# Optimization experiments

Measured on AMD Instinct MI355X. Metric: run time of the kernel, lower is better.

Reference implementation:

```python
import jax, jax.numpy as jnp
import numpy as np
from jax import lax

MAX_BOXES = 1000
IOU_THRESHOLD = 0.5
SCORE_THRESHOLD = 0.3
N_BOXES = 300000
N_FEAT = 85  # 4 box + 1 conf + 80 classes


def setup_inputs() -> dict:
    key = jax.random.key(0)
    inputs = jax.random.uniform(key, (N_BOXES, N_FEAT), dtype=jnp.float32)
    return {"inputs": inputs}


def _nms_indices(boxes, scores, max_boxes, iou_thr):
    """Fixed-size greedy NMS (tf.image.non_max_suppression semantics).
    Returns (idxs[max_boxes] int32, valid[max_boxes] bool). Padded slots invalid.
    Indices are non-differentiable, matching TF."""
    boxes = lax.stop_gradient(boxes)
    scores = lax.stop_gradient(scores)
    y1, x1, y2, x2 = boxes[:, 0], boxes[:, 1], boxes[:, 2], boxes[:, 3]
    areas = (y2 - y1) * (x2 - x1)

    def step(cur_scores, _):
        idx = jnp.argmax(cur_scores)
        valid = jnp.isfinite(cur_scores[idx])
        b = boxes[idx]
        iy1 = jnp.maximum(b[0], y1)
        ix1 = jnp.maximum(b[1], x1)
        iy2 = jnp.minimum(b[2], y2)
        ix2 = jnp.minimum(b[3], x2)
        inter = jnp.maximum(iy2 - iy1, 0.0) * jnp.maximum(ix2 - ix1, 0.0)
        union = areas[idx] + areas - inter
        iou = jnp.where(union > 0, inter / union, 0.0)
        suppress = (iou > iou_thr) & valid
        new_scores = jnp.where(suppress, -jnp.inf, cur_scores)
        new_scores = new_scores.at[idx].set(-jnp.inf)
        return new_scores, (idx.astype(jnp.int32), valid)

    _, (idxs, valids) = lax.scan(step, scores, None, length=max_boxes)
    return idxs, valids


def reference(inputs):
    boxes = inputs[..., 0:4]                      # [N,4]
    box_confidence = inputs[..., 4:5]             # [N,1]
    box_class_probs = inputs[..., 5:]             # [N,C]
    box_scores = box_confidence * box_class_probs # [N,C]
    box_classes = jnp.argmax(box_scores, axis=-1)        # [N]
    box_class_scores = jnp.max(box_scores, axis=-1)      # [N]
    # boolean_mask emulated by sending failing scores to -inf (fixed shape)
    keep = box_class_scores >= SCORE_THRESHOLD
    masked_scores = jnp.where(keep, box_class_scores, -jnp.inf)

    idxs, valids = _nms_indices(boxes, masked_scores, MAX_BOXES, IOU_THRESHOLD)

    out_boxes = boxes[idxs]                                  # [max_boxes,4]
    out_scores = box_class_scores[idxs][:, None]             # [max_boxes,1]
    out_classes = box_classes[idxs].astype(jnp.float32)[:, None]
    out = jnp.concatenate([out_boxes, out_classes, out_scores], axis=-1)  # [max_boxes,6]
    # zero padded (invalid) rows; original returned variable-length [k,6]
    return jnp.where(valids[:, None], out, 0.0)
```

## Files before the change

kernel.cpp:

```cpp
#include <hip/hip_runtime.h>

#define NBOX 300000
#define NFEAT 85
#define NCLS 80
#define NBUCK 4096
#define HSPLIT 16
#define CMAX 8192
#define W64 (CMAX / 64)
#define MAXKEEP 1000
#define SC_ROWS 64

typedef unsigned long long u64;
typedef float f4a __attribute__((ext_vector_type(4), aligned(16)));

__device__ __forceinline__ int bucket_of(float s) {
    int b = (int)((s - 0.3f) * (4096.0f / 0.7f));
    if (b < 0) b = 0;
    if (b > NBUCK - 1) b = NBUCK - 1;
    return b;
}

__device__ __forceinline__ bool sup_iou(float by1, float bx1, float by2, float bx2, float ba,
                                        float y1, float x1, float y2, float x2, float area) {
    float iy1 = fmaxf(by1, y1), ix1 = fmaxf(bx1, x1);
    float iy2 = fminf(by2, y2), ix2 = fminf(bx2, x2);
    float inter = fmaxf(iy2 - iy1, 0.0f) * fmaxf(ix2 - ix1, 0.0f);
    float uni = ba + area - inter;
    float iou = (uni > 0.0f) ? inter / uni : 0.0f;
    return iou > 0.5f;
}

__global__ void k_init(unsigned* __restrict__ hist16, unsigned* __restrict__ cnt,
                       int* __restrict__ meta) {
    int i = blockIdx.x * blockDim.x + threadIdx.x;
    if (i < HSPLIT * NBUCK) hist16[i] = 0u;
    if (i < NBUCK) cnt[i] = 0u;
    if (i < 16) meta[i] = 0;
}

__global__ void __launch_bounds__(256) k_scores(const float* __restrict__ in,
        float* __restrict__ scores, unsigned* __restrict__ hist16) {
    __shared__ float lds[SC_ROWS * NFEAT];
    int t = threadIdx.x;
    long long rbase = (long long)blockIdx.x * SC_ROWS;
    int rows = (NBOX - rbase < SC_ROWS) ? (int)(NBOX - rbase) : SC_ROWS;
    int nfl = rows * NFEAT;
    int nf4 = nfl >> 2;
    const f4a* src = (const f4a*)(in + rbase * NFEAT);
    f4a* dst = (f4a*)lds;
    for (int k = t; k < nf4; k += 256) dst[k] = src[k];
    for (int k = (nf4 << 2) + t; k < nfl; k += 256) lds[k] = in[rbase * NFEAT + k];
    __syncthreads();
    unsigned* myhist = hist16 + (size_t)(blockIdx.x & (HSPLIT - 1)) * NBUCK;
    int row = t >> 2, part = t & 3;
    if (row < rows) {
        const float* r = lds + row * NFEAT;
        const float* p = r + 5 + 20 * part;
        float mx = p[0];
        #pragma unroll
        for (int j = 1; j < 20; ++j) mx = fmaxf(mx, p[j]);
        mx = fmaxf(mx, __shfl_xor(mx, 1));
        mx = fmaxf(mx, __shfl_xor(mx, 2));
        if (part == 0) {
            float best = r[4] * mx;
            scores[rbase + row] = best;
            if (best >= 0.3f) atomicAdd(&myhist[bucket_of(best)], 1u);
        }
    }
}

__global__ void __launch_bounds__(1024) k_thresh(const unsigned* __restrict__ hist16,
        unsigned* __restrict__ histsum, unsigned* __restrict__ off, int* __restrict__ meta) {
    __shared__ unsigned chunk[1024];
    int t = threadIdx.x;
    unsigned h[4];
    unsigned s = 0;
    #pragma unroll
    for (int j = 0; j < 4; ++j) {
        unsigned v = 0;
        for (int g = 0; g < HSPLIT; ++g) v += hist16[g * NBUCK + t * 4 + j];
        h[j] = v; histsum[t * 4 + j] = v; s += v;
    }
    chunk[t] = s;
    __syncthreads();
    for (int o = 1; o < 1024; o <<= 1) {
        unsigned add = (t + o < 1024) ? chunk[t + o] : 0u;
        __syncthreads();
        chunk[t] += add;
        __syncthreads();
    }
    unsigned after = (t + 1 < 1024) ? chunk[t + 1] : 0u;
    unsigned suf[5];
    suf[4] = after;
    #pragma unroll
    for (int j = 3; j >= 0; --j) suf[j] = suf[j + 1] + h[j];
    #pragma unroll
    for (int j = 0; j < 4; ++j) {
        int b = t * 4 + j;
        off[b] = suf[j] - h[j];
        unsigned sufb = suf[j];
        unsigned sufprev;
        if (b == 0) sufprev = 0xFFFFFFFFu;
        else if (j > 0) sufprev = suf[j - 1];
        else {
            unsigned hprev = 0;
            for (int g = 0; g < HSPLIT; ++g) hprev += hist16[g * NBUCK + b - 1];
            sufprev = sufb + hprev;
        }
        if (sufb <= (unsigned)CMAX && sufprev > (unsigned)CMAX) {
            meta[1] = b;
            meta[0] = (int)sufb;
        }
    }
}

__global__ void k_scatter(const float* __restrict__ scores, const int* __restrict__ meta,
                          const unsigned* __restrict__ off, unsigned* __restrict__ cnt,
                          u64* __restrict__ unsorted) {
    int i = blockIdx.x * blockDim.x + threadIdx.x;
    if (i >= NBOX) return;
    float s = scores[i];
    if (s < 0.3f) return;
    int b = bucket_of(s);
    if (b < meta[1]) return;
    unsigned slot = off[b] + atomicAdd(&cnt[b], 1u);
    if (slot < CMAX)
        unsorted[slot] = ((u64)__float_as_uint(s) << 32) |
                         (u64)(0xFFFFFFFFu - (unsigned)i);
}

__global__ void k_rank(const float* __restrict__ in, const u64* __restrict__ unsorted,
                       const unsigned* __restrict__ off, const unsigned* __restrict__ histsum,
                       const int* __restrict__ meta, u64* __restrict__ sorted,
                       float4* __restrict__ boxes4, unsigned* __restrict__ vflag) {
    int i = blockIdx.x * blockDim.x + threadIdx.x;
    int total = meta[0];
    if (i >= total) return;
    u64 k = unsorted[i];
    float s = __uint_as_float((unsigned)(k >> 32));
    int b = bucket_of(s);
    unsigned base = off[b];
    unsigned n = histsum[b];
    unsigned r = 0;
    for (unsigned u = 0; u < n; ++u) r += (unsorted[base + u] > k) ? 1u : 0u;
    int bi = (int)(0xFFFFFFFFu - (unsigned)(k & 0xFFFFFFFFull));
    const float* p = in + (size_t)bi * NFEAT;
    float4 bx = make_float4(p[0], p[1], p[2], p[3]);
    sorted[base + r] = k;
    boxes4[base + r] = bx;
    vflag[base + r] = (bx.z > bx.x && bx.w > bx.y) ? 1u : 0u;
}

__global__ void __launch_bounds__(1024) k_vscan(const unsigned* __restrict__ vflag,
        const float4* __restrict__ boxes4, int* __restrict__ meta,
        unsigned* __restrict__ vincl, unsigned* __restrict__ cmap,
        float4* __restrict__ cboxes) {
    __shared__ unsigned ps[1024];
    int t = threadIdx.x;
    int total = meta[0];
    unsigned f[8];
    unsigned run = 0;
    #pragma unroll
    for (int e = 0; e < 8; ++e) {
        int s = t * 8 + e;
        unsigned v = (s < total) ? vflag[s] : 0u;
        run += v;
        f[e] = run;
    }
    ps[t] = run;
    __syncthreads();
    for (int o = 1; o < 1024; o <<= 1) {
        unsigned add = (t >= o) ? ps[t - o] : 0u;
        __syncthreads();
        ps[t] += add;
        __syncthreads();
    }
    unsigned excl = (t > 0) ? ps[t - 1] : 0u;
    #pragma unroll
    for (int e = 0; e < 8; ++e) {
        int s = t * 8 + e;
        unsigned incl = excl + f[e];
        vincl[s] = incl;
        if (s < total && vflag[s]) {
            cmap[incl - 1] = (unsigned)s;
            cboxes[incl - 1] = boxes4[s];
        }
    }
    if (t == 1023) meta[3] = (int)ps[1023];
}

__global__ void __launch_bounds__(256) k_masks(const float4* __restrict__ cboxes,
        const int* __restrict__ meta, u64* __restrict__ masks) {
    int ti = blockIdx.y, tj = blockIdx.x;
    if (tj < ti) return;
    int count = meta[3];
    if (ti * 64 >= count) return;
    __shared__ float4 rb[64];
    int t = threadIdx.x;
    if (t < 64) {
        int r = ti * 64 + t;
        rb[t] = (r < count) ? cboxes[r] : make_float4(0.f, 0.f, 0.f, 0.f);
    }
    int lane = t & 63, wid = t >> 6;
    int cj = tj * 64 + lane;
    bool cvalid = (cj < count);
    float4 cb = cvalid ? cboxes[cj] : make_float4(0.f, 0.f, 0.f, 0.f);
    float carea = (cb.z - cb.x) * (cb.w - cb.y);
    __syncthreads();
    #pragma unroll
    for (int r = 0; r < 16; ++r) {
        int i = ti * 64 + wid * 16 + r;
        float4 b = rb[wid * 16 + r];
        float ba = (b.z - b.x) * (b.w - b.y);
        bool s = cvalid && (cj > i) && (i < count) &&
                 sup_iou(b.x, b.y, b.z, b.w, ba, cb.x, cb.y, cb.z, cb.w, carea);
        u64 word = __ballot(s ? 1 : 0);
        if (lane == 0) masks[(size_t)i * W64 + tj] = word;
    }
}

__global__ void __launch_bounds__(1024) k_sweepfin(const u64* __restrict__ masks,
        const unsigned* __restrict__ cmap, const unsigned* __restrict__ vincl,
        const unsigned* __restrict__ vflag, int* __restrict__ meta,
        int* __restrict__ kfinal) {
    __shared__ __align__(16) u64 stage[2][64][130];
    __shared__ u64 vkeptw[W64];
    __shared__ unsigned ps[1024];
    __shared__ int sh_wlim;
    int t = threadIdx.x;
    if (t < W64) vkeptw[t] = 0ull;
    if (t == 0) sh_wlim = 0;
    __syncthreads();
    int total = meta[0];
    int nv = meta[3];

    if (t < 64) {
        int lane = t;
        int nblkv = (nv + 63) >> 6;
        u64 r0 = 0ull, r1 = 0ull;
        int nkv = 0, wl = 0;

        if (nblkv > 0) {
            #pragma unroll
            for (int k = 0; k < 64; ++k)
                __builtin_amdgcn_global_load_lds(
                    (const __attribute__((address_space(1))) void*)(masks + (size_t)k * W64 + 2 * lane),
                    (__attribute__((address_space(3))) void*)&stage[0][k][0], 16, 0, 0);
        }

        for (int w = 0; w < nblkv; ++w) {
            int buf = w & 1;
            int base = w << 6;
            int rc = nv - base;
            u64 vm = (rc >= 64) ? ~0ull : ((1ull << rc) - 1ull);
            u64 rw = __shfl((w & 1) ? r1 : r0, w >> 1);
            u64 surv = ~rw & vm;
            int cend = (base + 63 < nv - 1) ? (base + 63) : (nv - 1);
            unsigned cm = cmap[cend];
            bool more = (w + 1 < nblkv);
            int base2 = base + 64;

            if (more) {
                #pragma unroll
                for (int k = 0; k < 32; ++k)
                    __builtin_amdgcn_global_load_lds(
                        (const __attribute__((address_space(1))) void*)(masks + (size_t)(base2 + k) * W64 + 2 * lane),
                        (__attribute__((address_space(3))) void*)&stage[buf ^ 1][k][0], 16, 0, 0);
                asm volatile("s_waitcnt vmcnt(32)" ::: "memory");
            } else {
                asm volatile("s_waitcnt vmcnt(0)" ::: "memory");
            }
            __builtin_amdgcn_sched_barrier(0);

            u64 diag_cur = stage[buf][lane][w];
            u64 Z = __ballot(diag_cur == 0ull);
            u64 rem = 0ull;
            u64 mnz = surv & ~Z;
            while (mnz) {
                int b = __ffsll(mnz) - 1;
                mnz &= mnz - 1;
                if ((rem >> b) & 1ull) continue;
                u64 db = __shfl(diag_cur, b);
                rem |= db;
                mnz &= ~db;
            }
            u64 kept = surv & ~rem;
            int kp = __popcll(kept);

            if (more) {
                #pragma unroll
                for (int k = 32; k < 64; ++k)
                    __builtin_amdgcn_global_load_lds(
                        (const __attribute__((address_space(1))) void*)(masks + (size_t)(base2 + k) * W64 + 2 * lane),
                        (__attribute__((address_space(3))) void*)&stage[buf ^ 1][k][0], 16, 0, 0);
            }

            {
                u64 km = kept;
                u64 alo = 0ull, ahi = 0ull;
                while (km) {
                    int b = __ffsll(km) - 1;
                    km &= km - 1;
                    alo |= stage[buf][b][2 * lane];
                    ahi |= stage[buf][b][2 * lane + 1];
                }
                r0 |= alo; r1 |= ahi;
            }
            if (lane == 0) vkeptw[w] = kept;
            nkv += kp;
            wl = w + 1;
            if ((int)cm - cend + nkv >= MAXKEEP) break;
        }
        if (lane == 0) sh_wlim = wl;
    }
    __syncthreads();
    int wlim = sh_wlim;

    unsigned f[8];
    unsigned run = 0;
    #pragma unroll
    for (int e = 0; e < 8; ++e) {
        int s = t * 8 + e;
        unsigned kept = 0u;
        if (s < total) {
            if (!vflag[s]) kept = 1u;
            else {
                unsigned c = vincl[s] - 1u;
                int w = (int)(c >> 6);
                if (w < wlim && ((vkeptw[w] >> (c & 63u)) & 1ull)) kept = 1u;
            }
        }
        run += kept;
        f[e] = run;
    }
    ps[t] = run;
    __syncthreads();
    for (int o = 1; o < 1024; o <<= 1) {
        unsigned add = (t >= o) ? ps[t - o] : 0u;
        __syncthreads();
        ps[t] += add;
        __syncthreads();
    }
    unsigned excl = (t > 0) ? ps[t - 1] : 0u;
    #pragma unroll
    for (int e = 0; e < 8; ++e) {
        int s = t * 8 + e;
        unsigned kept = 0u;
        if (s < total) {
            if (!vflag[s]) kept = 1u;
            else {
                unsigned c = vincl[s] - 1u;
                int w = (int)(c >> 6);
                if (w < wlim && ((vkeptw[w] >> (c & 63u)) & 1ull)) kept = 1u;
            }
        }
        unsigned incl = excl + f[e];
        if (kept && incl <= (unsigned)MAXKEEP) kfinal[incl - 1] = s;
    }
    if (t == 1023) {
        unsigned tot = ps[1023];
        meta[2] = (int)(tot < (unsigned)MAXKEEP ? tot : (unsigned)MAXKEEP);
    }
}

__global__ void __launch_bounds__(256) k_output(const float* __restrict__ in,
        const u64* __restrict__ gkeys, const int* __restrict__ meta,
        const int* __restrict__ kfinal, float* __restrict__ out) {
    int gw = (blockIdx.x * blockDim.x + threadIdx.x) >> 6;
    int lane = threadIdx.x & 63;
    if (gw >= MAXKEEP) return;
    int kc = meta[2];
    if (gw < kc) {
        int pos = kfinal[gw];
        u64 key = gkeys[pos];
        int bi = (int)(0xFFFFFFFFu - (unsigned)(key & 0xFFFFFFFFull));
        const float* row = in + (size_t)bi * NFEAT;
        float conf = row[4];
        float v0 = (lane < NCLS) ? conf * row[5 + lane] : -1.0f;
        float v1 = (lane < NCLS - 64) ? conf * row[5 + 64 + lane] : -1.0f;
        float bv = (v1 > v0) ? v1 : v0;
        int bix = (v1 > v0) ? (64 + lane) : lane;
        #pragma unroll
        for (int o = 1; o < 64; o <<= 1) {
            float ov = __shfl_xor(bv, o);
            int oi = __shfl_xor(bix, o);
            if (ov > bv || (ov == bv && oi < bix)) { bv = ov; bix = oi; }
        }
        float wv = 0.f;
        if (lane < 4) wv = row[lane];
        else if (lane == 4) wv = (float)bix;
        else wv = bv;
        if (lane < 6) out[gw * 6 + lane] = wv;
    } else {
        if (lane < 6) out[gw * 6 + lane] = 0.f;
    }
}

extern "C" void kernel_launch(void* const* d_in, const int* in_sizes, int n_in,
                              void* d_out, int out_size, void* d_ws, size_t ws_size,
                              hipStream_t stream) {
    const float* in = (const float*)d_in[0];
    float* out = (float*)d_out;
    char* ws = (char*)d_ws;
    u64* sorted = (u64*)(ws);
    int* meta = (int*)(ws + 65536);
    int* kfinal = (int*)(ws + 65600);
    unsigned* vflag = (unsigned*)(ws + 69696);
    unsigned* vincl = (unsigned*)(ws + 102464);
    unsigned* cmap = (unsigned*)(ws + 135232);
    float4* cboxes = (float4*)(ws + 168000);
    float4* boxes4 = (float4*)(ws + 299072);
    u64* masks = (u64*)(ws + 430144);
    float* scores = (float*)(ws + 430144);
    unsigned* hist16 = (unsigned*)(ws + 1630144);
    unsigned* histsum = (unsigned*)(ws + 1892288);
    unsigned* cnt = (unsigned*)(ws + 1908672);
    unsigned* off = (unsigned*)(ws + 1925056);
    u64* unsorted = (u64*)(ws + 1941440);

    k_init<<<dim3(256), dim3(256), 0, stream>>>(hist16, cnt, meta);
    k_scores<<<dim3((NBOX + SC_ROWS - 1) / SC_ROWS), dim3(256), 0, stream>>>(in, scores, hist16);
    k_thresh<<<dim3(1), dim3(1024), 0, stream>>>(hist16, histsum, off, meta);
    k_scatter<<<dim3((NBOX + 255) / 256), dim3(256), 0, stream>>>(scores, meta, off, cnt, unsorted);
    k_rank<<<dim3(CMAX / 256), dim3(256), 0, stream>>>(in, unsorted, off, histsum, meta, sorted, boxes4, vflag);
    k_vscan<<<dim3(1), dim3(1024), 0, stream>>>(vflag, boxes4, meta, vincl, cmap, cboxes);
    k_masks<<<dim3(W64, W64), dim3(256), 0, stream>>>(cboxes, meta, masks);
    k_sweepfin<<<dim3(1), dim3(1024), 0, stream>>>(masks, cmap, vincl, vflag, meta, kfinal);
    k_output<<<dim3((MAXKEEP * 64 + 255) / 256), dim3(256), 0, stream>>>(in, sorted, meta, kfinal, out);
}
```

Before: 130.5 us.

## Merge post-score NMS stages into one cooperative kernel with grid syncs

Seven separate launches (threshold, scatter, rank, valid-scan, IoU masks, sweep, output) become one cooperative kernel of 256 blocks of 1024 threads, with grid.sync() between phases. If cooperative launch is unavailable, it falls back to separate launches. The mask phase now uses a wave-per-tile triangular schedule that broadcasts boxes with shuffles. The sweep drops its LDS double-buffered async staging and reads mask rows directly from global memory. This targets launch overhead and idle gaps between small kernels, at the cost of grid-wide barriers and possibly slower uncached mask reads in the serial sweep.

```diff
diff --git a/kernel.cpp b/kernel.cpp
--- a/kernel.cpp
+++ b/kernel.cpp
@@ -1,4 +1,7 @@
 #include <hip/hip_runtime.h>
+#include <hip/hip_cooperative_groups.h>
+
+namespace cg = cooperative_groups;
 
 #define NBOX 300000
 #define NFEAT 85
@@ -9,6 +12,8 @@
 #define W64 (CMAX / 64)
 #define MAXKEEP 1000
 #define SC_ROWS 64
+#define CB 256
+#define CT 1024
 
 typedef unsigned long long u64;
 typedef float f4a __attribute__((ext_vector_type(4), aligned(16)));
@@ -35,7 +40,7 @@
     int i = blockIdx.x * blockDim.x + threadIdx.x;
     if (i < HSPLIT * NBUCK) hist16[i] = 0u;
     if (i < NBUCK) cnt[i] = 0u;
-    if (i < 16) meta[i] = 0;
+    if (i < 48) meta[i] = 0;
 }
 
 __global__ void __launch_bounds__(256) k_scores(const float* __restrict__ in,
@@ -69,10 +74,10 @@
     }
 }
 
-__global__ void __launch_bounds__(1024) k_thresh(const unsigned* __restrict__ hist16,
-        unsigned* __restrict__ histsum, unsigned* __restrict__ off, int* __restrict__ meta) {
-    __shared__ unsigned chunk[1024];
-    int t = threadIdx.x;
+
+__device__ void phase_thresh(const unsigned* __restrict__ hist16,
+        unsigned* __restrict__ histsum, unsigned* __restrict__ off,
+        int* __restrict__ meta, unsigned* scan, int t) {
     unsigned h[4];
     unsigned s = 0;
     #pragma unroll
@@ -81,15 +86,15 @@
         for (int g = 0; g < HSPLIT; ++g) v += hist16[g * NBUCK + t * 4 + j];
         h[j] = v; histsum[t * 4 + j] = v; s += v;
     }
-    chunk[t] = s;
+    scan[t] = s;
     __syncthreads();
     for (int o = 1; o < 1024; o <<= 1) {
-        unsigned add = (t + o < 1024) ? chunk[t + o] : 0u;
-        __syncthreads();
-        chunk[t] += add;
-        __syncthreads();
-    }
-    unsigned after = (t + 1 < 1024) ? chunk[t + 1] : 0u;
+        unsigned add = (t + o < 1024) ? scan[t + o] : 0u;
+        __syncthreads();
+        scan[t] += add;
+        __syncthreads();
+    }
+    unsigned after = (t + 1 < 1024) ? scan[t + 1] : 0u;
     unsigned suf[5];
     suf[4] = after;
     #pragma unroll
@@ -98,8 +103,7 @@
     for (int j = 0; j < 4; ++j) {
         int b = t * 4 + j;
         off[b] = suf[j] - h[j];
-        unsigned sufb = suf[j];
-        unsigned sufprev;
+        unsigned sufb = suf[j], sufprev;
         if (b == 0) sufprev = 0xFFFFFFFFu;
         else if (j > 0) sufprev = suf[j - 1];
         else {
@@ -114,34 +118,33 @@
     }
 }
 
-__global__ void k_scatter(const float* __restrict__ scores, const int* __restrict__ meta,
-                          const unsigned* __restrict__ off, unsigned* __restrict__ cnt,
-                          u64* __restrict__ unsorted) {
-    int i = blockIdx.x * blockDim.x + threadIdx.x;
-    if (i >= NBOX) return;
-    float s = scores[i];
-    if (s < 0.3f) return;
-    int b = bucket_of(s);
-    if (b < meta[1]) return;
-    unsigned slot = off[b] + atomicAdd(&cnt[b], 1u);
-    if (slot < CMAX)
-        unsorted[slot] = ((u64)__float_as_uint(s) << 32) |
-                         (u64)(0xFFFFFFFFu - (unsigned)i);
-}
-
-__global__ void k_rank(const float* __restrict__ in, const u64* __restrict__ unsorted,
-                       const unsigned* __restrict__ off, const unsigned* __restrict__ histsum,
-                       const int* __restrict__ meta, u64* __restrict__ sorted,
-                       float4* __restrict__ boxes4, unsigned* __restrict__ vflag) {
-    int i = blockIdx.x * blockDim.x + threadIdx.x;
-    int total = meta[0];
+__device__ void phase_scatter(const float* __restrict__ scores, const int* meta,
+        const unsigned* __restrict__ off, unsigned* __restrict__ cnt,
+        u64* __restrict__ unsorted, int gtid, int gstride) {
+    int bstar = ((volatile const int*)meta)[1];
+    for (int i = gtid; i < NBOX; i += gstride) {
+        float s = scores[i];
+        if (s < 0.3f) continue;
+        int b = bucket_of(s);
+        if (b < bstar) continue;
+        unsigned slot = off[b] + atomicAdd(&cnt[b], 1u);
+        if (slot < CMAX)
+            unsorted[slot] = ((u64)__float_as_uint(s) << 32) |
+                             (u64)(0xFFFFFFFFu - (unsigned)i);
+    }
+}
+
+__device__ void phase_rank(const float* __restrict__ in, const u64* __restrict__ unsorted,
+        const unsigned* __restrict__ off, const unsigned* __restrict__ histsum,
+        const int* meta, u64* __restrict__ sorted, float4* __restrict__ boxes4,
+        unsigned* __restrict__ vflag, int gtid) {
+    int total = ((volatile const int*)meta)[0];
+    int i = gtid;
     if (i >= total) return;
     u64 k = unsorted[i];
     float s = __uint_as_float((unsigned)(k >> 32));
     int b = bucket_of(s);
-    unsigned base = off[b];
-    unsigned n = histsum[b];
-    unsigned r = 0;
+    unsigned base = off[b], n = histsum[b], r = 0;
     for (unsigned u = 0; u < n; ++u) r += (unsorted[base + u] > k) ? 1u : 0u;
     int bi = (int)(0xFFFFFFFFu - (unsigned)(k & 0xFFFFFFFFull));
     const float* p = in + (size_t)bi * NFEAT;
@@ -151,31 +154,28 @@
     vflag[base + r] = (bx.z > bx.x && bx.w > bx.y) ? 1u : 0u;
 }
 
-__global__ void __launch_bounds__(1024) k_vscan(const unsigned* __restrict__ vflag,
-        const float4* __restrict__ boxes4, int* __restrict__ meta,
-        unsigned* __restrict__ vincl, unsigned* __restrict__ cmap,
-        float4* __restrict__ cboxes) {
-    __shared__ unsigned ps[1024];
-    int t = threadIdx.x;
-    int total = meta[0];
+__device__ void phase_vscan(const unsigned* __restrict__ vflag,
+        const float4* __restrict__ boxes4, int* meta, unsigned* __restrict__ vincl,
+        unsigned* __restrict__ cmap, float4* __restrict__ cboxes,
+        unsigned* scan, int t) {
+    int total = ((volatile int*)meta)[0];
     unsigned f[8];
     unsigned run = 0;
     #pragma unroll
     for (int e = 0; e < 8; ++e) {
         int s = t * 8 + e;
         unsigned v = (s < total) ? vflag[s] : 0u;
-        run += v;
-        f[e] = run;
-    }
-    ps[t] = run;
+        run += v; f[e] = run;
+    }
+    scan[t] = run;
     __syncthreads();
     for (int o = 1; o < 1024; o <<= 1) {
-        unsigned add = (t >= o) ? ps[t - o] : 0u;
-        __syncthreads();
-        ps[t] += add;
-        __syncthreads();
-    }
-    unsigned excl = (t > 0) ? ps[t - 1] : 0u;
+        unsigned add = (t >= o) ? scan[t - o] : 0u;
+        __syncthreads();
+        scan[t] += add;
+        __syncthreads();
+    }
+    unsigned excl = (t > 0) ? scan[t - 1] : 0u;
     #pragma unroll
     for (int e = 0; e < 8; ++e) {
         int s = t * 8 + e;
@@ -186,70 +186,55 @@
             cboxes[incl - 1] = boxes4[s];
         }
     }
-    if (t == 1023) meta[3] = (int)ps[1023];
-}
-
-__global__ void __launch_bounds__(256) k_masks(const float4* __restrict__ cboxes,
-        const int* __restrict__ meta, u64* __restrict__ masks) {
-    int ti = blockIdx.y, tj = blockIdx.x;
-    if (tj < ti) return;
-    int count = meta[3];
-    if (ti * 64 >= count) return;
-    __shared__ float4 rb[64];
-    int t = threadIdx.x;
-    if (t < 64) {
-        int r = ti * 64 + t;
-        rb[t] = (r < count) ? cboxes[r] : make_float4(0.f, 0.f, 0.f, 0.f);
-    }
-    int lane = t & 63, wid = t >> 6;
-    int cj = tj * 64 + lane;
-    bool cvalid = (cj < count);
-    float4 cb = cvalid ? cboxes[cj] : make_float4(0.f, 0.f, 0.f, 0.f);
-    float carea = (cb.z - cb.x) * (cb.w - cb.y);
-    __syncthreads();
-    #pragma unroll
-    for (int r = 0; r < 16; ++r) {
-        int i = ti * 64 + wid * 16 + r;
-        float4 b = rb[wid * 16 + r];
-        float ba = (b.z - b.x) * (b.w - b.y);
-        bool s = cvalid && (cj > i) && (i < count) &&
-                 sup_iou(b.x, b.y, b.z, b.w, ba, cb.x, cb.y, cb.z, cb.w, carea);
-        u64 word = __ballot(s ? 1 : 0);
-        if (lane == 0) masks[(size_t)i * W64 + tj] = word;
-    }
-}
-
-__global__ void __launch_bounds__(1024) k_sweepfin(const u64* __restrict__ masks,
+    if (t == 1023) meta[16] = (int)scan[1023];
+}
+
+__device__ void phase_masks(const float4* __restrict__ cboxes, const int* meta,
+        u64* __restrict__ masks, int gwave, int nwaves, int lane) {
+    int nv = ((volatile const int*)meta)[16];
+    int nblk = (nv + 63) >> 6;
+    int T = nblk * (nblk + 1) / 2;
+    for (int tile = gwave; tile < T; tile += nwaves) {
+        int ti = 0, rem = tile, rowlen = nblk;
+        while (rem >= rowlen) { rem -= rowlen; --rowlen; ++ti; }
+        int tj = ti + rem;
+        int ri = ti * 64 + lane;
+        int cj = tj * 64 + lane;
+        float4 rb = (ri < nv) ? cboxes[ri] : make_float4(0.f, 0.f, 0.f, 0.f);
+        bool cvalid = (cj < nv);
+        float4 cb = cvalid ? cboxes[cj] : make_float4(0.f, 0.f, 0.f, 0.f);
+        float carea = (cb.z - cb.x) * (cb.w - cb.y);
+        u64 myw = 0ull;
+        for (int r = 0; r < 64; ++r) {
+            int i = ti * 64 + r;
+            float by1 = __shfl(rb.x, r), bx1 = __shfl(rb.y, r);
+            float by2 = __shfl(rb.z, r), bx2 = __shfl(rb.w, r);
+            float ba = (by2 - by1) * (bx2 - bx1);
+            bool s = cvalid && (cj > i) && (i < nv) &&
+                     sup_iou(by1, bx1, by2, bx2, ba, cb.x, cb.y, cb.z, cb.w, carea);
+            u64 word = __ballot(s ? 1 : 0);
+            if (lane == r) myw = word;
+        }
+        if (ri < nv) masks[(size_t)ri * W64 + tj] = myw;
+    }
+}
+
+__device__ void phase_sweepfin(const u64* __restrict__ masks,
         const unsigned* __restrict__ cmap, const unsigned* __restrict__ vincl,
-        const unsigned* __restrict__ vflag, int* __restrict__ meta,
-        int* __restrict__ kfinal) {
-    __shared__ __align__(16) u64 stage[2][64][130];
-    __shared__ u64 vkeptw[W64];
-    __shared__ unsigned ps[1024];
-    __shared__ int sh_wlim;
-    int t = threadIdx.x;
+        const unsigned* __restrict__ vflag, int* meta, int* __restrict__ kfinal,
+        unsigned* scan, u64* vkeptw, int* sh_wlim, int t) {
     if (t < W64) vkeptw[t] = 0ull;
-    if (t == 0) sh_wlim = 0;
-    __syncthreads();
-    int total = meta[0];
-    int nv = meta[3];
-
+    if (t == 0) *sh_wlim = 0;
+    __syncthreads();
+    int total = ((volatile int*)meta)[0];
+    int nv = ((volatile int*)meta)[16];
     if (t < 64) {
         int lane = t;
         int nblkv = (nv + 63) >> 6;
         u64 r0 = 0ull, r1 = 0ull;
         int nkv = 0, wl = 0;
-
-        if (nblkv > 0) {
-            #pragma unroll
-            for (int k = 0; k < 64; ++k)
-                __builtin_amdgcn_global_load_lds(
-                    (const __attribute__((address_space(1))) void*)(masks + (size_t)k * W64 + 2 * lane),
-                    (__attribute__((address_space(3))) void*)&stage[0][k][0], 16, 0, 0);
-        }
-
+        u64 diag_cur = (nblkv > 0) ? masks[(size_t)lane * W64] : 0ull;
         for (int w = 0; w < nblkv; ++w) {
-            int buf = w & 1;
             int base = w << 6;
             int rc = nv - base;
             u64 vm = (rc >= 64) ? ~0ull : ((1ull << rc) - 1ull);
@@ -257,65 +242,50 @@
             u64 surv = ~rw & vm;
             int cend = (base + 63 < nv - 1) ? (base + 63) : (nv - 1);
             unsigned cm = cmap[cend];
-            bool more = (w + 1 < nblkv);
-            int base2 = base + 64;
-
-            if (more) {
-                #pragma unroll
-                for (int k = 0; k < 32; ++k)
-                    __builtin_amdgcn_global_load_lds(
-                        (const __attribute__((address_space(1))) void*)(masks + (size_t)(base2 + k) * W64 + 2 * lane),
-                        (__attribute__((address_space(3))) void*)&stage[buf ^ 1][k][0], 16, 0, 0);
-                asm volatile("s_waitcnt vmcnt(32)" ::: "memory");
-            } else {
-                asm volatile("s_waitcnt vmcnt(0)" ::: "memory");
-            }
-            __builtin_amdgcn_sched_barrier(0);
-
-            u64 diag_cur = stage[buf][lane][w];
+            u64 diag_next = (w + 1 < nblkv)
+                ? masks[(size_t)((w + 1) * 64 + lane) * W64 + (w + 1)] : 0ull;
             u64 Z = __ballot(diag_cur == 0ull);
             u64 rem = 0ull;
             u64 mnz = surv & ~Z;
             while (mnz) {
-                int b = __ffsll(mnz) - 1;
+                int bb = __ffsll(mnz) - 1;
                 mnz &= mnz - 1;
-                if ((rem >> b) & 1ull) continue;
-                u64 db = __shfl(diag_cur, b);
+                if ((rem >> bb) & 1ull) continue;
+                u64 db = __shfl(diag_cur, bb);
                 rem |= db;
                 mnz &= ~db;
             }
             u64 kept = surv & ~rem;
             int kp = __popcll(kept);
-
-            if (more) {
-                #pragma unroll
-                for (int k = 32; k < 64; ++k)
-                    __builtin_amdgcn_global_load_lds(
-                        (const __attribute__((address_space(1))) void*)(masks + (size_t)(base2 + k) * W64 + 2 * lane),
-                        (__attribute__((address_space(3))) void*)&stage[buf ^ 1][k][0], 16, 0, 0);
+            u64 km = kept, alo = 0ull, ahi = 0ull;
+            while (km) {
+                int b0 = __ffsll(km) - 1; km &= km - 1;
+                const u64* p0 = masks + (size_t)(base + b0) * W64 + 2 * lane;
+                u64 l0 = p0[0], h0 = p0[1];
+                u64 l1 = 0, h1 = 0, l2 = 0, h2 = 0, l3 = 0, h3 = 0;
+                if (km) { int b = __ffsll(km) - 1; km &= km - 1;
+                    const u64* p = masks + (size_t)(base + b) * W64 + 2 * lane;
+                    l1 = p[0]; h1 = p[1]; }
+                if (km) { int b = __ffsll(km) - 1; km &= km - 1;
+                    const u64* p = masks + (size_t)(base + b) * W64 + 2 * lane;
+                    l2 = p[0]; h2 = p[1]; }
+                if (km) { int b = __ffsll(km) - 1; km &= km - 1;
+                    const u64* p = masks + (size_t)(base + b) * W64 + 2 * lane;
+                    l3 = p[0]; h3 = p[1]; }
+                alo |= l0 | l1 | l2 | l3;
+                ahi |= h0 | h1 | h2 | h3;
             }
-
-            {
-                u64 km = kept;
-                u64 alo = 0ull, ahi = 0ull;
-                while (km) {
-                    int b = __ffsll(km) - 1;
-                    km &= km - 1;
-                    alo |= stage[buf][b][2 * lane];
-                    ahi |= stage[buf][b][2 * lane + 1];
-                }
-                r0 |= alo; r1 |= ahi;
-            }
+            r0 |= alo; r1 |= ahi;
             if (lane == 0) vkeptw[w] = kept;
             nkv += kp;
             wl = w + 1;
             if ((int)cm - cend + nkv >= MAXKEEP) break;
-        }
-        if (lane == 0) sh_wlim = wl;
-    }
-    __syncthreads();
-    int wlim = sh_wlim;
-
+            diag_cur = diag_next;
+        }
+        if (lane == 0) *sh_wlim = wl;
+    }
+    __syncthreads();
+    int wlim = *sh_wlim;
     unsigned f[8];
     unsigned run = 0;
     #pragma unroll
@@ -330,18 +300,17 @@
                 if (w < wlim && ((vkeptw[w] >> (c & 63u)) & 1ull)) kept = 1u;
             }
         }
-        run += kept;
-        f[e] = run;
-    }
-    ps[t] = run;
+        run += kept; f[e] = run;
+    }
+    scan[t] = run;
     __syncthreads();
     for (int o = 1; o < 1024; o <<= 1) {
-        unsigned add = (t >= o) ? ps[t - o] : 0u;
-        __syncthreads();
-        ps[t] += add;
-        __syncthreads();
-    }
-    unsigned excl = (t > 0) ? ps[t - 1] : 0u;
+        unsigned add = (t >= o) ? scan[t - o] : 0u;
+        __syncthreads();
+        scan[t] += add;
+        __syncthreads();
+    }
+    unsigned excl = (t > 0) ? scan[t - 1] : 0u;
     #pragma unroll
     for (int e = 0; e < 8; ++e) {
         int s = t * 8 + e;
@@ -358,21 +327,19 @@
         if (kept && incl <= (unsigned)MAXKEEP) kfinal[incl - 1] = s;
     }
     if (t == 1023) {
-        unsigned tot = ps[1023];
-        meta[2] = (int)(tot < (unsigned)MAXKEEP ? tot : (unsigned)MAXKEEP);
-    }
-}
-
-__global__ void __launch_bounds__(256) k_output(const float* __restrict__ in,
-        const u64* __restrict__ gkeys, const int* __restrict__ meta,
-        const int* __restrict__ kfinal, float* __restrict__ out) {
-    int gw = (blockIdx.x * blockDim.x + threadIdx.x) >> 6;
-    int lane = threadIdx.x & 63;
-    if (gw >= MAXKEEP) return;
-    int kc = meta[2];
-    if (gw < kc) {
-        int pos = kfinal[gw];
-        u64 key = gkeys[pos];
+        unsigned tot = scan[1023];
+        meta[32] = (int)(tot < (unsigned)MAXKEEP ? tot : (unsigned)MAXKEEP);
+    }
+}
+
+__device__ void phase_output(const float* __restrict__ in, const u64* __restrict__ sorted,
+        const int* meta, const int* __restrict__ kfinal, float* __restrict__ out,
+        int gwave, int lane) {
+    if (gwave >= MAXKEEP) return;
+    int kc = ((volatile const int*)meta)[32];
+    if (gwave < kc) {
+        int pos = kfinal[gwave];
+        u64 key = sorted[pos];
         int bi = (int)(0xFFFFFFFFu - (unsigned)(key & 0xFFFFFFFFull));
         const float* row = in + (size_t)bi * NFEAT;
         float conf = row[4];
@@ -390,10 +357,80 @@
         if (lane < 4) wv = row[lane];
         else if (lane == 4) wv = (float)bix;
         else wv = bv;
-        if (lane < 6) out[gw * 6 + lane] = wv;
+        if (lane < 6) out[gwave * 6 + lane] = wv;
     } else {
-        if (lane < 6) out[gw * 6 + lane] = 0.f;
-    }
+        if (lane < 6) out[gwave * 6 + lane] = 0.f;
+    }
+}
+
+__global__ void __launch_bounds__(CT) k_coop(const float* in, float* scores,
+        unsigned* hist16, unsigned* histsum, unsigned* off, unsigned* cnt,
+        u64* unsorted, u64* sorted, float4* boxes4, unsigned* vflag,
+        unsigned* vincl, unsigned* cmap, float4* cboxes, u64* masks,
+        int* meta, int* kfinal, float* out) {
+    cg::grid_group grid = cg::this_grid();
+    __shared__ unsigned scan[1024];
+    __shared__ u64 vkeptw[W64];
+    __shared__ int sh_wlim;
+    int t = threadIdx.x, b = blockIdx.x;
+    int gtid = b * CT + t;
+    int lane = t & 63;
+    int gwave = gtid >> 6;
+    if (b == 0) phase_thresh(hist16, histsum, off, meta, scan, t);
+    grid.sync();
+    phase_scatter(scores, meta, off, cnt, unsorted, gtid, CB * CT);
+    grid.sync();
+    phase_rank(in, unsorted, off, histsum, meta, sorted, boxes4, vflag, gtid);
+    grid.sync();
+    if (b == 0) phase_vscan(vflag, boxes4, meta, vincl, cmap, cboxes, scan, t);
+    grid.sync();
+    phase_masks(cboxes, meta, masks, gwave, CB * 16, lane);
+    grid.sync();
+    if (b == 0) phase_sweepfin(masks, cmap, vincl, vflag, meta, kfinal, scan, vkeptw, &sh_wlim, t);
+    grid.sync();
+    phase_output(in, sorted, meta, kfinal, out, gwave, lane);
+}
+
+__global__ void __launch_bounds__(1024) k_thresh_s(const unsigned* hist16,
+        unsigned* histsum, unsigned* off, int* meta) {
+    __shared__ unsigned scan[1024];
+    phase_thresh(hist16, histsum, off, meta, scan, threadIdx.x);
+}
+__global__ void k_scatter_s(const float* scores, const int* meta, const unsigned* off,
+        unsigned* cnt, u64* unsorted) {
+    phase_scatter(scores, meta, off, cnt, unsorted,
+                  blockIdx.x * 256 + threadIdx.x, 1172 * 256);
+}
+__global__ void k_rank_s(const float* in, const u64* unsorted, const unsigned* off,
+        const unsigned* histsum, const int* meta, u64* sorted, float4* boxes4,
+        unsigned* vflag) {
+    phase_rank(in, unsorted, off, histsum, meta, sorted, boxes4, vflag,
+               blockIdx.x * 256 + threadIdx.x);
+}
+__global__ void __launch_bounds__(1024) k_vscan_s(const unsigned* vflag,
+        const float4* boxes4, int* meta, unsigned* vincl, unsigned* cmap,
+        float4* cboxes) {
+    __shared__ unsigned scan[1024];
+    phase_vscan(vflag, boxes4, meta, vincl, cmap, cboxes, scan, threadIdx.x);
+}
+__global__ void __launch_bounds__(1024) k_masks_s(const float4* cboxes,
+        const int* meta, u64* masks) {
+    int gwave = blockIdx.x * 16 + (threadIdx.x >> 6);
+    phase_masks(cboxes, meta, masks, gwave, 64 * 16, threadIdx.x & 63);
+}
+__global__ void __launch_bounds__(1024) k_sweepfin_s(const u64* masks,
+        const unsigned* cmap, const unsigned* vincl, const unsigned* vflag,
+        int* meta, int* kfinal) {
+    __shared__ unsigned scan[1024];
+    __shared__ u64 vkeptw[W64];
+    __shared__ int sh_wlim;
+    phase_sweepfin(masks, cmap, vincl, vflag, meta, kfinal, scan, vkeptw,
+                   &sh_wlim, threadIdx.x);
+}
+__global__ void __launch_bounds__(1024) k_output_s(const float* in, const u64* sorted,
+        const int* meta, const int* kfinal, float* out) {
+    int gwave = blockIdx.x * 16 + (threadIdx.x >> 6);
+    phase_output(in, sorted, meta, kfinal, out, gwave, threadIdx.x & 63);
 }
 
 extern "C" void kernel_launch(void* const* d_in, const int* in_sizes, int n_in,
@@ -404,27 +441,47 @@
     char* ws = (char*)d_ws;
     u64* sorted = (u64*)(ws);
     int* meta = (int*)(ws + 65536);
-    int* kfinal = (int*)(ws + 65600);
-    unsigned* vflag = (unsigned*)(ws + 69696);
-    unsigned* vincl = (unsigned*)(ws + 102464);
-    unsigned* cmap = (unsigned*)(ws + 135232);
-    float4* cboxes = (float4*)(ws + 168000);
-    float4* boxes4 = (float4*)(ws + 299072);
-    u64* masks = (u64*)(ws + 430144);
-    float* scores = (float*)(ws + 430144);
-    unsigned* hist16 = (unsigned*)(ws + 1630144);
-    unsigned* histsum = (unsigned*)(ws + 1892288);
-    unsigned* cnt = (unsigned*)(ws + 1908672);
-    unsigned* off = (unsigned*)(ws + 1925056);
-    u64* unsorted = (u64*)(ws + 1941440);
+    int* kfinal = (int*)(ws + 65728);
+    unsigned* vflag = (unsigned*)(ws + 69824);
+    unsigned* vincl = (unsigned*)(ws + 102592);
+    unsigned* cmap = (unsigned*)(ws + 135360);
+    float4* cboxes = (float4*)(ws + 168128);
+    float4* boxes4 = (float4*)(ws + 299200);
+    u64* masks = (u64*)(ws + 430272);
+    float* scores = (float*)(ws + 430272);
+    unsigned* hist16 = (unsigned*)(ws + 1630272);
+    unsigned* histsum = (unsigned*)(ws + 1892416);
+    unsigned* cnt = (unsigned*)(ws + 1908800);
+    unsigned* off = (unsigned*)(ws + 1925184);
+    u64* unsorted = (u64*)(ws + 1941568);
 
     k_init<<<dim3(256), dim3(256), 0, stream>>>(hist16, cnt, meta);
     k_scores<<<dim3((NBOX + SC_ROWS - 1) / SC_ROWS), dim3(256), 0, stream>>>(in, scores, hist16);
-    k_thresh<<<dim3(1), dim3(1024), 0, stream>>>(hist16, histsum, off, meta);
-    k_scatter<<<dim3((NBOX + 255) / 256), dim3(256), 0, stream>>>(scores, meta, off, cnt, unsorted);
-    k_rank<<<dim3(CMAX / 256), dim3(256), 0, stream>>>(in, unsorted, off, histsum, meta, sorted, boxes4, vflag);
-    k_vscan<<<dim3(1), dim3(1024), 0, stream>>>(vflag, boxes4, meta, vincl, cmap, cboxes);
-    k_masks<<<dim3(W64, W64), dim3(256), 0, stream>>>(cboxes, meta, masks);
-    k_sweepfin<<<dim3(1), dim3(1024), 0, stream>>>(masks, cmap, vincl, vflag, meta, kfinal);
-    k_output<<<dim3((MAXKEEP * 64 + 255) / 256), dim3(256), 0, stream>>>(in, sorted, meta, kfinal, out);
-}
+
+    int dev = 0;
+    (void)hipGetDevice(&dev);
+    int coopAttr = 0;
+    (void)hipDeviceGetAttribute(&coopAttr, hipDeviceAttributeCooperativeLaunch, dev);
+    int maxb = 0;
+    hipError_t occErr = hipOccupancyMaxActiveBlocksPerMultiprocessor(&maxb, k_coop, CT, 0);
+    bool useCoop = (coopAttr != 0) && (occErr == hipSuccess) && (maxb >= 1);
+    if (useCoop) {
+        void* kp[17] = { (void*)&in, (void*)&scores, (void*)&hist16, (void*)&histsum,
+                         (void*)&off, (void*)&cnt, (void*)&unsorted, (void*)&sorted,
+                         (void*)&boxes4, (void*)&vflag, (void*)&vincl, (void*)&cmap,
+                         (void*)&cboxes, (void*)&masks, (void*)&meta, (void*)&kfinal,
+                         (void*)&out };
+        hipError_t e = hipLaunchCooperativeKernel((const void*)k_coop,
+                dim3(CB), dim3(CT), kp, 0, stream);
+        if (e != hipSuccess) useCoop = false;
+    }
+    if (!useCoop) {
+        k_thresh_s<<<dim3(1), dim3(1024), 0, stream>>>(hist16, histsum, off, meta);
+        k_scatter_s<<<dim3(1172), dim3(256), 0, stream>>>(scores, meta, off, cnt, unsorted);
+        k_rank_s<<<dim3(32), dim3(256), 0, stream>>>(in, unsorted, off, histsum, meta, sorted, boxes4, vflag);
+        k_vscan_s<<<dim3(1), dim3(1024), 0, stream>>>(vflag, boxes4, meta, vincl, cmap, cboxes);
+        k_masks_s<<<dim3(64), dim3(1024), 0, stream>>>(cboxes, meta, masks);
+        k_sweepfin_s<<<dim3(1), dim3(1024), 0, stream>>>(masks, cmap, vincl, vflag, meta, kfinal);
+        k_output_s<<<dim3(63), dim3(1024), 0, stream>>>(in, sorted, meta, kfinal, out);
+    }
+}
```

After: 143.2 us. +9.7%, slower.

## Replace LDS-staged mask blocks with direct sparse global loads in NMS sweep

Applied to the files above, without the earlier changes.

The sweep kernel no longer double-buffers full 64-row mask blocks into LDS with async global_load_lds. It instead loads only the diagonal word per block, prefetched one iteration ahead, and reads the rows of kept boxes straight from global memory, unrolled four at a time. This cuts bytes moved when few boxes are kept per block and frees about 130KB of LDS. In exchange, global-load latency now sits on the serial critical path of the single-wave sweep.

```diff
diff --git a/kernel.cpp b/kernel.cpp
--- a/kernel.cpp
+++ b/kernel.cpp
@@ -98,8 +98,7 @@
     for (int j = 0; j < 4; ++j) {
         int b = t * 4 + j;
         off[b] = suf[j] - h[j];
-        unsigned sufb = suf[j];
-        unsigned sufprev;
+        unsigned sufb = suf[j], sufprev;
         if (b == 0) sufprev = 0xFFFFFFFFu;
         else if (j > 0) sufprev = suf[j - 1];
         else {
@@ -223,9 +222,8 @@
         const unsigned* __restrict__ cmap, const unsigned* __restrict__ vincl,
         const unsigned* __restrict__ vflag, int* __restrict__ meta,
         int* __restrict__ kfinal) {
-    __shared__ __align__(16) u64 stage[2][64][130];
+    __shared__ unsigned scan[1024];
     __shared__ u64 vkeptw[W64];
-    __shared__ unsigned ps[1024];
     __shared__ int sh_wlim;
     int t = threadIdx.x;
     if (t < W64) vkeptw[t] = 0ull;
@@ -239,17 +237,8 @@
         int nblkv = (nv + 63) >> 6;
         u64 r0 = 0ull, r1 = 0ull;
         int nkv = 0, wl = 0;
-
-        if (nblkv > 0) {
-            #pragma unroll
-            for (int k = 0; k < 64; ++k)
-                __builtin_amdgcn_global_load_lds(
-                    (const __attribute__((address_space(1))) void*)(masks + (size_t)k * W64 + 2 * lane),
-                    (__attribute__((address_space(3))) void*)&stage[0][k][0], 16, 0, 0);
-        }
-
+        u64 diag_cur = (nblkv > 0) ? masks[(size_t)lane * W64] : 0ull;
         for (int w = 0; w < nblkv; ++w) {
-            int buf = w & 1;
             int base = w << 6;
             int rc = nv - base;
             u64 vm = (rc >= 64) ? ~0ull : ((1ull << rc) - 1ull);
@@ -257,59 +246,45 @@
             u64 surv = ~rw & vm;
             int cend = (base + 63 < nv - 1) ? (base + 63) : (nv - 1);
             unsigned cm = cmap[cend];
-            bool more = (w + 1 < nblkv);
-            int base2 = base + 64;
-
-            if (more) {
-                #pragma unroll
-                for (int k = 0; k < 32; ++k)
-                    __builtin_amdgcn_global_load_lds(
-                        (const __attribute__((address_space(1))) void*)(masks + (size_t)(base2 + k) * W64 + 2 * lane),
-                        (__attribute__((address_space(3))) void*)&stage[buf ^ 1][k][0], 16, 0, 0);
-                asm volatile("s_waitcnt vmcnt(32)" ::: "memory");
-            } else {
-                asm volatile("s_waitcnt vmcnt(0)" ::: "memory");
-            }
-            __builtin_amdgcn_sched_barrier(0);
-
-            u64 diag_cur = stage[buf][lane][w];
+            u64 diag_next = (w + 1 < nblkv)
+                ? masks[(size_t)((w + 1) * 64 + lane) * W64 + (w + 1)] : 0ull;
             u64 Z = __ballot(diag_cur == 0ull);
             u64 rem = 0ull;
             u64 mnz = surv & ~Z;
             while (mnz) {
-                int b = __ffsll(mnz) - 1;
+                int bb = __ffsll(mnz) - 1;
                 mnz &= mnz - 1;
-                if ((rem >> b) & 1ull) continue;
-                u64 db = __shfl(diag_cur, b);
+                if ((rem >> bb) & 1ull) continue;
+                u64 db = __shfl(diag_cur, bb);
                 rem |= db;
                 mnz &= ~db;
             }
             u64 kept = surv & ~rem;
             int kp = __popcll(kept);
-
-            if (more) {
-                #pragma unroll
-                for (int k = 32; k < 64; ++k)
-                    __builtin_amdgcn_global_load_lds(
-                        (const __attribute__((address_space(1))) void*)(masks + (size_t)(base2 + k) * W64 + 2 * lane),
-                        (__attribute__((address_space(3))) void*)&stage[buf ^ 1][k][0], 16, 0, 0);
+            u64 km = kept, alo = 0ull, ahi = 0ull;
+            while (km) {
+                int b0 = __ffsll(km) - 1; km &= km - 1;
+                const u64* p0 = masks + (size_t)(base + b0) * W64 + 2 * lane;
+                u64 l0 = p0[0], h0 = p0[1];
+                u64 l1 = 0, h1 = 0, l2 = 0, h2 = 0, l3 = 0, h3 = 0;
+                if (km) { int b = __ffsll(km) - 1; km &= km - 1;
+                    const u64* p = masks + (size_t)(base + b) * W64 + 2 * lane;
+                    l1 = p[0]; h1 = p[1]; }
+                if (km) { int b = __ffsll(km) - 1; km &= km - 1;
+                    const u64* p = masks + (size_t)(base + b) * W64 + 2 * lane;
+                    l2 = p[0]; h2 = p[1]; }
+                if (km) { int b = __ffsll(km) - 1; km &= km - 1;
+                    const u64* p = masks + (size_t)(base + b) * W64 + 2 * lane;
+                    l3 = p[0]; h3 = p[1]; }
+                alo |= l0 | l1 | l2 | l3;
+                ahi |= h0 | h1 | h2 | h3;
             }
-
-            {
-                u64 km = kept;
-                u64 alo = 0ull, ahi = 0ull;
-                while (km) {
-                    int b = __ffsll(km) - 1;
-                    km &= km - 1;
-                    alo |= stage[buf][b][2 * lane];
-                    ahi |= stage[buf][b][2 * lane + 1];
-                }
-                r0 |= alo; r1 |= ahi;
-            }
+            r0 |= alo; r1 |= ahi;
             if (lane == 0) vkeptw[w] = kept;
             nkv += kp;
             wl = w + 1;
             if ((int)cm - cend + nkv >= MAXKEEP) break;
+            diag_cur = diag_next;
         }
         if (lane == 0) sh_wlim = wl;
     }
@@ -333,15 +308,15 @@
         run += kept;
         f[e] = run;
     }
-    ps[t] = run;
+    scan[t] = run;
     __syncthreads();
     for (int o = 1; o < 1024; o <<= 1) {
-        unsigned add = (t >= o) ? ps[t - o] : 0u;
-        __syncthreads();
-        ps[t] += add;
-        __syncthreads();
-    }
-    unsigned excl = (t > 0) ? ps[t - 1] : 0u;
+        unsigned add = (t >= o) ? scan[t - o] : 0u;
+        __syncthreads();
+        scan[t] += add;
+        __syncthreads();
+    }
+    unsigned excl = (t > 0) ? scan[t - 1] : 0u;
     #pragma unroll
     for (int e = 0; e < 8; ++e) {
         int s = t * 8 + e;
@@ -358,7 +333,7 @@
         if (kept && incl <= (unsigned)MAXKEEP) kfinal[incl - 1] = s;
     }
     if (t == 1023) {
-        unsigned tot = ps[1023];
+        unsigned tot = scan[1023];
         meta[2] = (int)(tot < (unsigned)MAXKEEP ? tot : (unsigned)MAXKEEP);
     }
 }
```

Measured after the change: 134.3 us. 1.03x slower.
